# Performance work log

Hardware: AMD Instinct MI355X
Metric: run time of the kernel (lower is better)

## Reference

```python
import jax, jax.numpy as jnp
import numpy as np

K = 9  # ATSS top-k candidates per GT


def cxcywh_to_xyxy(b):
    cx, cy, w, h = b[..., 0], b[..., 1], b[..., 2], b[..., 3]
    return jnp.stack([cx - 0.5 * w, cy - 0.5 * h, cx + 0.5 * w, cy + 0.5 * h], axis=-1)


def elementwise_iou(a, b):
    # a, b: [..., 4] xyxy, broadcastable
    lt = jnp.maximum(a[..., :2], b[..., :2])
    rb = jnp.minimum(a[..., 2:], b[..., 2:])
    wh = jnp.clip(rb - lt, 0.0)
    inter = wh[..., 0] * wh[..., 1]
    area_a = (a[..., 2] - a[..., 0]) * (a[..., 3] - a[..., 1])
    area_b = (b[..., 2] - b[..., 0]) * (b[..., 3] - b[..., 1])
    return inter / (area_a + area_b - inter)


def setup_inputs() -> dict:
    key = jax.random.key(0)
    k1, k2 = jax.random.split(key)
    pred_boxes = jax.random.uniform(k1, (16, 30000, 4), dtype=jnp.float32)
    gt_boxes = jax.random.uniform(k2, (16, 64, 4), dtype=jnp.float32)
    return {"pred_boxes": pred_boxes, "gt_boxes": gt_boxes}


def reference(pred_boxes, gt_boxes):
    # pred_boxes: [B, N, 4] cxcywh; gt_boxes: [B, G, 4] cxcywh
    G = gt_boxes.shape[1]

    def per_image(pred, gt):
        # center-distance matrix [G, N] (the cdist in the original)
        diff = gt[:, None, :2] - pred[None, :, :2]
        dist = jnp.sqrt(jnp.sum(diff * diff, axis=-1))
        # k smallest distances per GT
        _, k_idx = jax.lax.top_k(-dist, K)          # [G, K]
        k_boxes = pred[k_idx]                        # [G, K, 4]
        gt_xyxy = cxcywh_to_xyxy(gt)                 # [G, 4]
        kb_xyxy = cxcywh_to_xyxy(k_boxes)            # [G, K, 4]
        ious = elementwise_iou(gt_xyxy[:, None, :], kb_xyxy)  # [G, K]
        # adaptive threshold: mean + std (torch.std is unbiased -> ddof=1)
        thr = jnp.mean(ious, axis=1, keepdims=True) + jnp.std(ious, axis=1, ddof=1, keepdims=True)
        cx, cy = k_boxes[..., 0], k_boxes[..., 1]
        inside = ((gt_xyxy[:, None, 0] <= cx) & (cx <= gt_xyxy[:, None, 2]) &
                  (gt_xyxy[:, None, 1] <= cy) & (cy <= gt_xyxy[:, None, 3]))
        mask = (ious >= thr) & inside                # [G, K]
        # padded index representation (original returns ragged lists):
        pred_idx = jnp.where(mask, k_idx, -1)
        gt_idx = jnp.where(mask, jnp.arange(G, dtype=jnp.int64)[:, None], -1)
        return pred_idx, gt_idx, mask, ious

    return jax.vmap(per_image)(pred_boxes, gt_boxes)
```

## Files before the change

### kernel.cpp

```cpp
#include <hip/hip_runtime.h>
#include <stdint.h>

typedef unsigned long long u64;

#define KCAND 9
#define BATCH 16
#define NPRED 30000
#define NGT   64
#define TPB   256
#define UNR   8
#define NT    15
#define INITKEY 0x7F800000FFFFFFFFULL

__device__ __forceinline__ u64 wave_min_u64(u64 v) {
#pragma unroll
    for (int s = 1; s < 64; s <<= 1) {
        u64 o = __shfl_xor(v, s, 64);
        v = o < v ? o : v;
    }
    return v;
}

__global__ __launch_bounds__(256) void compact_xy(
    const float* __restrict__ pred, float2* __restrict__ xy)
{
    int e = blockIdx.x * 256 + threadIdx.x;
    if (e < BATCH * NPRED) {
        float4 p = ((const float4*)pred)[e];
        xy[e] = make_float2(p.x, p.y);
    }
}

template <int S2>
__global__ __launch_bounds__(TPB, 4) void atss_kernel(
    const float2* __restrict__ xy,
    const float*  __restrict__ pred,
    const float*  __restrict__ gt,
    float* __restrict__ out)
{
#pragma clang fp contract(off)
    const int tid  = threadIdx.x;
    const int lane = tid & 63;
    const int wvid = tid >> 6;

    const int b = (blockIdx.x & 7) + 8 * (blockIdx.x >> 9);
    const int g = (blockIdx.x >> 3) & 63;
    const int w = b * NGT + g;

    const float4 gtb = ((const float4*)gt)[w];
    const float gcx = gtb.x, gcy = gtb.y;
    const float2* xyb   = xy + (size_t)b * NPRED * S2;
    const float4* pred4 = (const float4*)pred + (size_t)b * NPRED;

    u64 val = INITKEY;
    float Tf = __uint_as_float(0x7F800000u);

    for (int t = 0; t < NT; ++t) {
        const int i0 = t * (TPB * UNR) + wvid * (64 * UNR) + lane;
        float d2[UNR];
#pragma unroll
        for (int j = 0; j < UNR; ++j) {
            const int i = i0 + j * 64;
            const bool v = i < NPRED;
            float2 p = xyb[(v ? i : 0) * S2];
            float dx = __fsub_rn(gcx, p.x);
            float dy = __fsub_rn(gcy, p.y);
            float d = __fadd_rn(__fmul_rn(dx, dx), __fmul_rn(dy, dy));
            d2[j] = v ? d : __uint_as_float(0x7F800000u);
        }
        float dmin = d2[0];
#pragma unroll
        for (int j = 1; j < UNR; ++j) dmin = fminf(dmin, d2[j]);
        if (__ballot(dmin <= Tf) == 0ULL) continue;

#pragma unroll
        for (int j = 0; j < UNR; ++j) {
            u64 pend = __ballot(d2[j] <= Tf);
            while (pend) {
                const int src = __ffsll(pend) - 1;
                pend &= pend - 1;
                const unsigned kd = __shfl(__float_as_uint(d2[j]), src, 64);
                const unsigned ki = (unsigned)(i0 + j * 64 - lane + src);
                const u64 key = ((u64)kd << 32) | ki;
                u64 Tkey = __shfl(val, 8, 64);
                if (key < Tkey) {
                    const u64 ltm = __ballot(val < key) & 0x1FFULL;
                    const int pos = __popcll(ltm);
                    const u64 sh = __shfl_up(val, 1, 64);
                    if (lane < KCAND) {
                        if (lane == pos)      val = key;
                        else if (lane > pos)  val = sh;
                    }
                    Tkey = __shfl(val, 8, 64);
                    Tf = __uint_as_float((unsigned)(Tkey >> 32));
                    pend &= __ballot(d2[j] <= Tf);
                }
            }
        }
    }

    __shared__ u64 smem[4 * KCAND];
    if (lane < KCAND) smem[wvid * KCAND + lane] = val;
    __syncthreads();

    if (wvid != 0) return;

    u64 key = (lane < 4 * KCAND) ? smem[lane] : ~0ULL;
    u64 fin = 0;
#pragma unroll
    for (int k = 0; k < KCAND; ++k) {
        u64 m = wave_min_u64(key);
        if (lane == k) fin = m;
        if (key == m) key = ~0ULL;
    }

    const bool active = (lane < KCAND);
    const unsigned idx = active ? (unsigned)(fin & 0xffffffffu) : 0u;

    float4 pb = pred4[idx];

    float gx1 = gcx - 0.5f * gtb.z, gy1 = gcy - 0.5f * gtb.w;
    float gx2 = gcx + 0.5f * gtb.z, gy2 = gcy + 0.5f * gtb.w;
    float kx1 = pb.x - 0.5f * pb.z, ky1 = pb.y - 0.5f * pb.w;
    float kx2 = pb.x + 0.5f * pb.z, ky2 = pb.y + 0.5f * pb.w;

    float ltx = fmaxf(gx1, kx1), lty = fmaxf(gy1, ky1);
    float rbx = fminf(gx2, kx2), rby = fminf(gy2, ky2);
    float wvd = fmaxf(rbx - ltx, 0.0f);
    float hvd = fmaxf(rby - lty, 0.0f);
    float inter  = wvd * hvd;
    float area_a = (gx2 - gx1) * (gy2 - gy1);
    float area_b = (kx2 - kx1) * (ky2 - ky1);
    float iou = inter / ((area_a + area_b) - inter);

    float v = active ? iou : 0.0f;
    float s = v;
#pragma unroll
    for (int m = 1; m < 64; m <<= 1) s += __shfl_xor(s, m, 64);
    float mean = s / 9.0f;

    float dev = active ? (iou - mean) : 0.0f;
    float ss = dev * dev;
#pragma unroll
    for (int m = 1; m < 64; m <<= 1) ss += __shfl_xor(ss, m, 64);
    float stdv = sqrtf(ss / 8.0f);
    float thr = mean + stdv;

    bool inside = (gx1 <= pb.x) && (pb.x <= gx2) &&
                  (gy1 <= pb.y) && (pb.y <= gy2);
    bool maskk = (iou >= thr) && inside;

    if (active) {
        const size_t chunk = (size_t)BATCH * NGT * KCAND;
        const size_t o = (size_t)w * KCAND + lane;
        out[0 * chunk + o] = maskk ? (float)idx : -1.0f;
        out[1 * chunk + o] = maskk ? (float)g   : -1.0f;
        out[2 * chunk + o] = maskk ? 1.0f : 0.0f;
        out[3 * chunk + o] = iou;
    }
}

extern "C" void kernel_launch(void* const* d_in, const int* in_sizes, int n_in,
                              void* d_out, int out_size, void* d_ws, size_t ws_size,
                              hipStream_t stream) {
    const float* pred = (const float*)d_in[0];
    const float* gtb  = (const float*)d_in[1];
    float* out = (float*)d_out;

    const size_t need = (size_t)BATCH * NPRED * sizeof(float2);
    if (ws_size >= need) {
        float2* xy = (float2*)d_ws;
        compact_xy<<<(BATCH * NPRED + 255) / 256, 256, 0, stream>>>(pred, xy);
        atss_kernel<1><<<BATCH * NGT, TPB, 0, stream>>>(xy, pred, gtb, out);
    } else {
        atss_kernel<2><<<BATCH * NGT, TPB, 0, stream>>>(
            (const float2*)pred, pred, gtb, out);
    }
}
```

Baseline: 97.49 us.

## Prepass threshold from per-lane minima and keep top-k in uniform registers

Adds a first pass computing per-lane minimum distances, then bitonic-sorts them across the wave to obtain a tight initial threshold (9th smallest of distinct-point minima). The top-9 list is kept as scalar-uniform registers updated by a compare-swap chain instead of lane-distributed ballot/shuffle insertion, and the final cross-wave merge uses the same scheme. This aims to cut the number of insertions and their shuffle cost, at the price of reading the distance data twice.

```diff
diff --git a/kernel.cpp b/kernel.cpp
--- a/kernel.cpp
+++ b/kernel.cpp
@@ -11,15 +11,7 @@
 #define UNR   8
 #define NT    15
 #define INITKEY 0x7F800000FFFFFFFFULL
-
-__device__ __forceinline__ u64 wave_min_u64(u64 v) {
-#pragma unroll
-    for (int s = 1; s < 64; s <<= 1) {
-        u64 o = __shfl_xor(v, s, 64);
-        v = o < v ? o : v;
-    }
-    return v;
-}
+#define FINF __uint_as_float(0x7F800000u)
 
 __global__ __launch_bounds__(256) void compact_xy(
     const float* __restrict__ pred, float2* __restrict__ xy)
@@ -28,6 +20,21 @@
     if (e < BATCH * NPRED) {
         float4 p = ((const float4*)pred)[e];
         xy[e] = make_float2(p.x, p.y);
+    }
+}
+
+template <int S2, bool MASK>
+__device__ __forceinline__ void load_d2(const float2* __restrict__ xyb, int i0,
+                                        float gcx, float gcy, float (&d2)[UNR]) {
+#pragma unroll
+    for (int j = 0; j < UNR; ++j) {
+        const int i = i0 + j * 64;
+        const bool v = !MASK || (i < NPRED);
+        float2 p = xyb[(v ? i : 0) * S2];
+        float dx = __fsub_rn(gcx, p.x);
+        float dy = __fsub_rn(gcy, p.y);
+        float d  = __fadd_rn(__fmul_rn(dx, dx), __fmul_rn(dy, dy));
+        d2[j] = v ? d : FINF;
     }
 }
 
@@ -52,67 +59,123 @@
     const float2* xyb   = xy + (size_t)b * NPRED * S2;
     const float4* pred4 = (const float4*)pred + (size_t)b * NPRED;
 
-    u64 val = INITKEY;
-    float Tf = __uint_as_float(0x7F800000u);
-
-    for (int t = 0; t < NT; ++t) {
-        const int i0 = t * (TPB * UNR) + wvid * (64 * UNR) + lane;
-        float d2[UNR];
-#pragma unroll
-        for (int j = 0; j < UNR; ++j) {
-            const int i = i0 + j * 64;
-            const bool v = i < NPRED;
-            float2 p = xyb[(v ? i : 0) * S2];
-            float dx = __fsub_rn(gcx, p.x);
-            float dy = __fsub_rn(gcy, p.y);
-            float d = __fadd_rn(__fmul_rn(dx, dx), __fmul_rn(dy, dy));
-            d2[j] = v ? d : __uint_as_float(0x7F800000u);
-        }
-        float dmin = d2[0];
-#pragma unroll
-        for (int j = 1; j < UNR; ++j) dmin = fminf(dmin, d2[j]);
-        if (__ballot(dmin <= Tf) == 0ULL) continue;
-
-#pragma unroll
-        for (int j = 0; j < UNR; ++j) {
-            u64 pend = __ballot(d2[j] <= Tf);
-            while (pend) {
-                const int src = __ffsll(pend) - 1;
-                pend &= pend - 1;
-                const unsigned kd = __shfl(__float_as_uint(d2[j]), src, 64);
-                const unsigned ki = (unsigned)(i0 + j * 64 - lane + src);
-                const u64 key = ((u64)kd << 32) | ki;
-                u64 Tkey = __shfl(val, 8, 64);
-                if (key < Tkey) {
-                    const u64 ltm = __ballot(val < key) & 0x1FFULL;
-                    const int pos = __popcll(ltm);
-                    const u64 sh = __shfl_up(val, 1, 64);
-                    if (lane < KCAND) {
-                        if (lane == pos)      val = key;
-                        else if (lane > pos)  val = sh;
-                    }
-                    Tkey = __shfl(val, 8, 64);
-                    Tf = __uint_as_float((unsigned)(Tkey >> 32));
-                    pend &= __ballot(d2[j] <= Tf);
-                }
+    const int ibase0 = wvid * (64 * UNR) + lane;
+
+    float lmin = FINF;
+    for (int t = 0; t < NT - 1; ++t) {
+        float d2[UNR];
+        load_d2<S2, false>(xyb, t * (TPB * UNR) + ibase0, gcx, gcy, d2);
+#pragma unroll
+        for (int j = 0; j < UNR; ++j) lmin = fminf(lmin, d2[j]);
+    }
+    {
+        float d2[UNR];
+        load_d2<S2, true>(xyb, (NT - 1) * (TPB * UNR) + ibase0, gcx, gcy, d2);
+#pragma unroll
+        for (int j = 0; j < UNR; ++j) lmin = fminf(lmin, d2[j]);
+    }
+
+    {
+        float x = lmin;
+#pragma unroll
+        for (int k = 2; k <= 64; k <<= 1) {
+#pragma unroll
+            for (int j = k >> 1; j >= 1; j >>= 1) {
+                float o = __shfl_xor(x, j, 64);
+                bool keepmin = (((lane & k) == 0) == ((lane & j) == 0));
+                x = keepmin ? fminf(x, o) : fmaxf(x, o);
             }
         }
+        lmin = x;
+    }
+    float Tf = __uint_as_float((unsigned)__builtin_amdgcn_readlane(
+                                   (int)__float_as_uint(lmin), 8));
+
+    u64 t0=INITKEY,t1=INITKEY,t2=INITKEY,t3=INITKEY,t4=INITKEY,
+        t5=INITKEY,t6=INITKEY,t7=INITKEY,t8=INITKEY;
+
+#define SW(T) { bool c_ = x < (T); u64 lo_ = c_ ? x : (T); u64 hi_ = c_ ? (T) : x; (T) = lo_; x = hi_; }
+#define SWAP9 SW(t0) SW(t1) SW(t2) SW(t3) SW(t4) SW(t5) SW(t6) SW(t7) SW(t8)
+
+#define PROCESS(I0) { \
+    float dmin = d2[0]; \
+    _Pragma("unroll") \
+    for (int j = 1; j < UNR; ++j) dmin = fminf(dmin, d2[j]); \
+    if (__ballot(dmin <= Tf) != 0ULL) { \
+        _Pragma("unroll") \
+        for (int j = 0; j < UNR; ++j) { \
+            u64 pend = __ballot(d2[j] <= Tf); \
+            while (pend) { \
+                const int src = __ffsll(pend) - 1; \
+                pend &= pend - 1; \
+                const unsigned kd = (unsigned)__builtin_amdgcn_readlane( \
+                                        (int)__float_as_uint(d2[j]), src); \
+                const unsigned ki = (unsigned)((I0) - lane + j * 64 + src); \
+                u64 key = ((u64)kd << 32) | ki; \
+                if (key < t8) { \
+                    u64 x = key; SWAP9; \
+                    Tf = fminf(Tf, __uint_as_float((unsigned)(t8 >> 32))); \
+                    pend &= __ballot(d2[j] <= Tf); \
+                } \
+            } \
+        } \
+    } }
+
+    for (int t = 0; t < NT - 1; ++t) {
+        const int i0 = t * (TPB * UNR) + ibase0;
+        float d2[UNR];
+        load_d2<S2, false>(xyb, i0, gcx, gcy, d2);
+        PROCESS(i0)
+    }
+    {
+        const int i0 = (NT - 1) * (TPB * UNR) + ibase0;
+        float d2[UNR];
+        load_d2<S2, true>(xyb, i0, gcx, gcy, d2);
+        PROCESS(i0)
     }
 
     __shared__ u64 smem[4 * KCAND];
-    if (lane < KCAND) smem[wvid * KCAND + lane] = val;
+    if (lane == 0) {
+        u64* s = smem + wvid * KCAND;
+        s[0]=t0; s[1]=t1; s[2]=t2; s[3]=t3; s[4]=t4;
+        s[5]=t5; s[6]=t6; s[7]=t7; s[8]=t8;
+    }
     __syncthreads();
 
     if (wvid != 0) return;
 
-    u64 key = (lane < 4 * KCAND) ? smem[lane] : ~0ULL;
-    u64 fin = 0;
-#pragma unroll
-    for (int k = 0; k < KCAND; ++k) {
-        u64 m = wave_min_u64(key);
-        if (lane == k) fin = m;
-        if (key == m) key = ~0ULL;
-    }
+    u64 cand = (lane < 4 * KCAND) ? smem[lane] : INITKEY;
+    const float cd = __uint_as_float((unsigned)(cand >> 32));
+    t0=INITKEY;t1=INITKEY;t2=INITKEY;t3=INITKEY;t4=INITKEY;
+    t5=INITKEY;t6=INITKEY;t7=INITKEY;t8=INITKEY;
+    Tf = FINF;
+    {
+        u64 pend = __ballot(cd < FINF);
+        while (pend) {
+            const int src = __ffsll(pend) - 1;
+            pend &= pend - 1;
+            const unsigned kd = (unsigned)__builtin_amdgcn_readlane(
+                                    (int)(unsigned)(cand >> 32), src);
+            const unsigned ki = (unsigned)__builtin_amdgcn_readlane(
+                                    (int)(unsigned)cand, src);
+            u64 key = ((u64)kd << 32) | ki;
+            if (key < t8) {
+                u64 x = key; SWAP9;
+                Tf = fminf(Tf, __uint_as_float((unsigned)(t8 >> 32)));
+                pend &= __ballot(cd <= Tf);
+            }
+        }
+    }
+
+    u64 fin = t0;
+    if (lane == 1) fin = t1;
+    if (lane == 2) fin = t2;
+    if (lane == 3) fin = t3;
+    if (lane == 4) fin = t4;
+    if (lane == 5) fin = t5;
+    if (lane == 6) fin = t6;
+    if (lane == 7) fin = t7;
+    if (lane == 8) fin = t8;
 
     const bool active = (lane < KCAND);
     const unsigned idx = active ? (unsigned)(fin & 0xffffffffu) : 0u;
@@ -158,6 +221,9 @@
         out[2 * chunk + o] = maskk ? 1.0f : 0.0f;
         out[3 * chunk + o] = iou;
     }
+#undef PROCESS
+#undef SWAP9
+#undef SW
 }
 
 extern "C" void kernel_launch(void* const* d_in, const int* in_sizes, int n_in,
@@ -169,9 +235,9 @@
 
     const size_t need = (size_t)BATCH * NPRED * sizeof(float2);
     if (ws_size >= need) {
-        float2* xy = (float2*)d_ws;
-        compact_xy<<<(BATCH * NPRED + 255) / 256, 256, 0, stream>>>(pred, xy);
-        atss_kernel<1><<<BATCH * NGT, TPB, 0, stream>>>(xy, pred, gtb, out);
+        float2* xyc = (float2*)d_ws;
+        compact_xy<<<(BATCH * NPRED + 255) / 256, 256, 0, stream>>>(pred, xyc);
+        atss_kernel<1><<<BATCH * NGT, TPB, 0, stream>>>(xyc, pred, gtb, out);
     } else {
         atss_kernel<2><<<BATCH * NGT, TPB, 0, stream>>>(
             (const float2*)pred, pred, gtb, out);
```

Measured after the change: 99.70 us. 2.3% more time.
